# Kernel optimization log

Measured on AMD Instinct MI355X. Metric: run time of the kernel, lower is better.

The kernel has to match this reference:

```python
import jax, jax.numpy as jnp
import numpy as np

DIM = 768
B, N = 16, 1024
EPS_LN = 1e-5

def _layernorm(x, gamma, beta):
    mu = jnp.mean(x, axis=-1, keepdims=True)
    var = jnp.mean((x - mu) ** 2, axis=-1, keepdims=True)
    return (x - mu) * jax.lax.rsqrt(var + EPS_LN) * gamma + beta

def _gelu(x):
    return jax.nn.gelu(x, approximate=False)

def setup_inputs() -> dict:
    key = jax.random.key(0)
    ks = jax.random.split(key, 10)
    d = DIM
    s1 = 1.0 / np.sqrt(2 * d)
    s = 1.0 / np.sqrt(d)
    return {
        "x": jax.random.normal(ks[0], (B, N, d), dtype=jnp.float32),
        "gamma": jnp.ones((d,), jnp.float32),
        "beta": jnp.zeros((d,), jnp.float32),
        "w1": jax.random.normal(ks[1], (2 * d, d), jnp.float32) * s1,
        "b1": jnp.zeros((d,), jnp.float32),
        "w2": jax.random.normal(ks[2], (d, d), jnp.float32) * s,
        "b2": jnp.zeros((d,), jnp.float32),
        "w3": jax.random.normal(ks[3], (d, d), jnp.float32) * s,
        "b3": jnp.zeros((d,), jnp.float32),
        "w4": jax.random.normal(ks[4], (d, d), jnp.float32) * s,
        "b4": jnp.zeros((d,), jnp.float32),
    }

def reference(x, gamma, beta, w1, b1, w2, b2, w3, b3, w4, b4):
    # x: [B, N, D]
    avg_x = jnp.mean(x, axis=1)                      # [B, D]
    A = avg_x[:, None, :] * jax.nn.sigmoid(_layernorm(x, gamma, beta))  # [B, N, D]
    # batched pairwise Euclidean distance among tokens (replaces python loop)
    sq = jnp.sum(A * A, axis=-1)                     # [B, N]
    d2 = sq[:, :, None] + sq[:, None, :] - 2.0 * jnp.einsum('bnd,bmd->bnm', A, A)
    dist = jnp.sqrt(jnp.clip(d2, 1e-12))             # [B, N, N]
    m = jnp.max(dist, axis=-1)                       # [B, N]
    m_x = x + m[..., None]                           # [B, N, D]
    cat = jnp.concatenate([A, m_x], axis=-1)         # [B, N, 2D]
    m1 = _gelu(cat @ w1 + b1)                        # layer1
    W = _gelu(m1 @ w2 + b2)                          # layer2
    Wdyn = x * W
    l3 = _gelu((m1 * Wdyn) @ w3 + b3)                # layer3
    out = _gelu((x * l3) @ w4 + b4)                  # layer4
    return out.astype(jnp.float32)
```

## Files before the change

kernel.cpp:

```cpp
#include <hip/hip_runtime.h>
#include <hip/hip_fp16.h>
#include <math.h>

#define DIM 768
#define NTOK 1024
#define NBATCH 16
#define BNR (NBATCH * NTOK)

typedef _Float16 f16x8 __attribute__((ext_vector_type(8)));
typedef float f32x4 __attribute__((ext_vector_type(4)));

__device__ __forceinline__ void gl2lds16(const void* g, void* l) {
    __builtin_amdgcn_global_load_lds(
        (const __attribute__((address_space(1))) void*)g,
        (__attribute__((address_space(3))) void*)l, 16, 0, 0);
}

__device__ __forceinline__ float gelu_fast(float z) {
    const float s = z * 0.70710678118654752f;
    const float ax = fabsf(s);
    const float t = __builtin_amdgcn_rcpf(1.0f + 0.3275911f * ax);
    const float poly = t * (0.254829592f + t * (-0.284496736f +
                       t * (1.421413741f + t * (-1.453152027f + t * 1.061405429f))));
    const float e = __expf(-ax * ax);
    float erfv = 1.0f - poly * e;
    erfv = copysignf(erfv, s);
    return 0.5f * z * (1.0f + erfv);
}

__device__ __forceinline__ float block_sum(float v, float* sbuf) {
    #pragma unroll
    for (int o = 32; o > 0; o >>= 1) v += __shfl_down(v, o, 64);
    const int lane = threadIdx.x & 63, w = threadIdx.x >> 6;
    if (lane == 0) sbuf[w] = v;
    __syncthreads();
    const float r = sbuf[0] + sbuf[1] + sbuf[2] + sbuf[3];
    __syncthreads();
    return r;
}

__global__ __launch_bounds__(256) void avg_kernel(const float* __restrict__ x,
                                                  float* __restrict__ avgx) {
    const int d = blockIdx.x * 256 + threadIdx.x;
    const int b = blockIdx.y;
    const int n0 = blockIdx.z * 128;
    const float* xp = x + (size_t)b * NTOK * DIM + (size_t)n0 * DIM + d;
    float s = 0.0f;
    for (int n = 0; n < 128; ++n) s += xp[(size_t)n * DIM];
    atomicAdd(&avgx[b * DIM + d], s * (1.0f / NTOK));
}

__global__ __launch_bounds__(256) void ln_sig_kernel(
    const float* __restrict__ x, const float* __restrict__ gamma,
    const float* __restrict__ beta, const float* __restrict__ avgx,
    __half* __restrict__ Ah, float* __restrict__ sq)
{
    __shared__ float sbuf[4];
    const int row = blockIdx.x;
    const int b = row >> 10;
    const int tid = threadIdx.x;
    const float* xr = x + (size_t)row * DIM;
    float v[3];
    #pragma unroll
    for (int i = 0; i < 3; ++i) v[i] = xr[tid + 256 * i];
    const float mu = block_sum(v[0] + v[1] + v[2], sbuf) * (1.0f / DIM);
    float ss = 0.0f;
    #pragma unroll
    for (int i = 0; i < 3; ++i) { const float d = v[i] - mu; ss += d * d; }
    const float var = block_sum(ss, sbuf) * (1.0f / DIM);
    const float rstd = rsqrtf(var + 1e-5f);
    const float* ag = avgx + b * DIM;
    float qs = 0.0f;
    #pragma unroll
    for (int i = 0; i < 3; ++i) {
        const int d = tid + 256 * i;
        const float ln = (v[i] - mu) * rstd * gamma[d] + beta[d];
        const float sg = 1.0f / (1.0f + expf(-ln));
        const float a = ag[d] * sg;
        const __half h = __float2half(a);
        const float ar = __half2float(h);
        Ah[(size_t)row * DIM + d] = h;
        qs += ar * ar;
    }
    const float tot = block_sum(qs, sbuf);
    if (tid == 0) sq[row] = tot;
}

__global__ __launch_bounds__(256) void wconv(const float* __restrict__ w,
                                             __half* __restrict__ wT, int K, int N)
{
    __shared__ float t[64][65];
    const int k0 = blockIdx.y * 64, n0 = blockIdx.x * 64;
    const int tid = threadIdx.x;
    const int r = tid >> 4, c4 = (tid & 15) * 4;
    #pragma unroll
    for (int p = 0; p < 4; ++p) {
        const int rr = p * 16 + r;
        const float4 v = *(const float4*)&w[(size_t)(k0 + rr) * N + n0 + c4];
        t[rr][c4] = v.x; t[rr][c4 + 1] = v.y; t[rr][c4 + 2] = v.z; t[rr][c4 + 3] = v.w;
    }
    __syncthreads();
    #pragma unroll
    for (int p = 0; p < 4; ++p) {
        const int nn = p * 16 + r;
        ushort4 pk;
        pk.x = __half_as_ushort(__float2half(t[c4 + 0][nn]));
        pk.y = __half_as_ushort(__float2half(t[c4 + 1][nn]));
        pk.z = __half_as_ushort(__float2half(t[c4 + 2][nn]));
        pk.w = __half_as_ushort(__float2half(t[c4 + 3][nn]));
        *(ushort4*)&wT[(size_t)(n0 + nn) * K + k0 + c4] = pk;
    }
}

__global__ __launch_bounds__(256) void xm_kernel(const float* __restrict__ x,
                                                 const float* __restrict__ m,
                                                 __half* __restrict__ xmH) {
    const int row = blockIdx.x;
    const float mv = m[row];
    #pragma unroll
    for (int i = 0; i < 3; ++i) {
        const int d = threadIdx.x + i * 256;
        xmH[(size_t)row * DIM + d] = __float2half(x[(size_t)row * DIM + d] + mv);
    }
}

template<int K, bool CAT, int EPI>
__global__ __launch_bounds__(256, 4) void gemm16(
    const __half* __restrict__ A0, const __half* __restrict__ A1,
    const __half* __restrict__ BT, const float* __restrict__ bias,
    const float* __restrict__ xin, const __half* __restrict__ m1h,
    __half* __restrict__ outH, float* __restrict__ outF)
{
    __shared__ _Float16 As0[128 * 32];
    __shared__ _Float16 Bs0[128 * 32];
    __shared__ _Float16 As1[128 * 32];
    __shared__ _Float16 Bs1[128 * 32];
    const int tid = threadIdx.x;
    const int w = tid >> 6, lane = tid & 63;
    const int wu = __builtin_amdgcn_readfirstlane(w);
    const int wr = w >> 1, wc = w & 1;
    const int R0 = blockIdx.x * 128, J0 = blockIdx.y * 128;
    constexpr int rs = CAT ? DIM : K;
    const int srow = lane >> 2;
    const int sk8 = (((lane & 3) ^ ((lane >> 2) & 3))) * 8;
    const int fx = ((lane >> 4) ^ (lane & 3)) * 8;
    constexpr int NT = K / 32;
    static_assert(NT % 2 == 0, "two-phase loop needs even NT");

    f32x4 acc[4][4];
    #pragma unroll
    for (int mt = 0; mt < 4; ++mt)
        #pragma unroll
        for (int nt = 0; nt < 4; ++nt) {
            f32x4 z = {0.0f, 0.0f, 0.0f, 0.0f};
            acc[mt][nt] = z;
        }

    auto stage = [&](_Float16 (&Asb)[128 * 32], _Float16 (&Bsb)[128 * 32], int k0) {
        const __half* Ab = (CAT && k0 >= DIM) ? (A1 + (k0 - DIM)) : (A0 + k0);
        #pragma unroll
        for (int i = 0; i < 2; ++i) {
            const int rbase = i * 64 + w * 16;
            const int rbu = i * 64 + wu * 16;
            gl2lds16(Ab + (size_t)(R0 + rbase + srow) * rs + sk8, &Asb[rbu * 32]);
            gl2lds16(BT + (size_t)(J0 + rbase + srow) * K + k0 + sk8, &Bsb[rbu * 32]);
        }
    };
    auto rdfrags = [&](const _Float16 (&Asb)[128 * 32], const _Float16 (&Bsb)[128 * 32],
                       f16x8* af, f16x8* bf) {
        #pragma unroll
        for (int mt = 0; mt < 4; ++mt)
            af[mt] = *(const f16x8*)&Asb[(wr * 64 + mt * 16 + (lane & 15)) * 32 + fx];
        #pragma unroll
        for (int nt = 0; nt < 4; ++nt)
            bf[nt] = *(const f16x8*)&Bsb[(wc * 64 + nt * 16 + (lane & 15)) * 32 + fx];
    };
    auto domfma = [&](const f16x8* af, const f16x8* bf) {
        #pragma unroll
        for (int mt = 0; mt < 4; ++mt)
            #pragma unroll
            for (int nt = 0; nt < 4; ++nt)
                acc[mt][nt] = __builtin_amdgcn_mfma_f32_16x16x32_f16(af[mt], bf[nt], acc[mt][nt], 0, 0, 0);
    };

    stage(As0, Bs0, 0);
    __syncthreads();
    for (int kt = 0; kt < NT; kt += 2) {
        f16x8 af[4], bf[4];
        rdfrags(As0, Bs0, af, bf);
        stage(As1, Bs1, (kt + 1) * 32);
        domfma(af, bf);
        __syncthreads();
        rdfrags(As1, Bs1, af, bf);
        if (kt + 2 < NT) stage(As0, Bs0, (kt + 2) * 32);
        domfma(af, bf);
        __syncthreads();
    }

    #pragma unroll
    for (int mt = 0; mt < 4; ++mt) {
        #pragma unroll
        for (int nt = 0; nt < 4; ++nt) {
            const int col = J0 + wc * 64 + nt * 16 + (lane & 15);
            const float bv = bias[col];
            #pragma unroll
            for (int r = 0; r < 4; ++r) {
                const int row = R0 + wr * 64 + mt * 16 + (lane >> 4) * 4 + r;
                const size_t off = (size_t)row * DIM + col;
                const float g = gelu_fast(acc[mt][nt][r] + bv);
                if (EPI == 0) {
                    outH[off] = __float2half(g);
                } else if (EPI == 1) {
                    outH[off] = __float2half(__half2float(m1h[off]) * xin[off] * g);
                } else if (EPI == 2) {
                    outH[off] = __float2half(xin[off] * g);
                } else {
                    outF[off] = g;
                }
            }
        }
    }
}

__global__ __launch_bounds__(256, 4) void dist16(const __half* __restrict__ Ah,
                                                 const float* __restrict__ sq,
                                                 float* __restrict__ m)
{
    __shared__ _Float16 As0[128 * 32];
    __shared__ _Float16 Bs0[128 * 32];
    __shared__ _Float16 As1[128 * 32];
    __shared__ _Float16 Bs1[128 * 32];
    const int tid = threadIdx.x;
    const int w = tid >> 6, lane = tid & 63;
    const int wu = __builtin_amdgcn_readfirstlane(w);
    const int wr = w >> 1, wc = w & 1;
    const int base = blockIdx.x * NTOK;
    const int I0 = blockIdx.y * 128, J0 = blockIdx.z * 128;
    const int srow = lane >> 2;
    const int sk8 = (((lane & 3) ^ ((lane >> 2) & 3))) * 8;
    const int fx = ((lane >> 4) ^ (lane & 3)) * 8;
    constexpr int NT = DIM / 32;

    f32x4 acc[4][4];
    #pragma unroll
    for (int mt = 0; mt < 4; ++mt)
        #pragma unroll
        for (int nt = 0; nt < 4; ++nt) {
            f32x4 z = {0.0f, 0.0f, 0.0f, 0.0f};
            acc[mt][nt] = z;
        }

    auto stage = [&](_Float16 (&Asb)[128 * 32], _Float16 (&Bsb)[128 * 32], int k0) {
        #pragma unroll
        for (int i = 0; i < 2; ++i) {
            const int rbase = i * 64 + w * 16;
            const int rbu = i * 64 + wu * 16;
            gl2lds16(Ah + (size_t)(base + I0 + rbase + srow) * DIM + k0 + sk8, &Asb[rbu * 32]);
            gl2lds16(Ah + (size_t)(base + J0 + rbase + srow) * DIM + k0 + sk8, &Bsb[rbu * 32]);
        }
    };
    auto rdfrags = [&](const _Float16 (&Asb)[128 * 32], const _Float16 (&Bsb)[128 * 32],
                       f16x8* af, f16x8* bf) {
        #pragma unroll
        for (int mt = 0; mt < 4; ++mt)
            af[mt] = *(const f16x8*)&Asb[(wr * 64 + mt * 16 + (lane & 15)) * 32 + fx];
        #pragma unroll
        for (int nt = 0; nt < 4; ++nt)
            bf[nt] = *(const f16x8*)&Bsb[(wc * 64 + nt * 16 + (lane & 15)) * 32 + fx];
    };
    auto domfma = [&](const f16x8* af, const f16x8* bf) {
        #pragma unroll
        for (int mt = 0; mt < 4; ++mt)
            #pragma unroll
            for (int nt = 0; nt < 4; ++nt)
                acc[mt][nt] = __builtin_amdgcn_mfma_f32_16x16x32_f16(af[mt], bf[nt], acc[mt][nt], 0, 0, 0);
    };

    stage(As0, Bs0, 0);
    __syncthreads();
    for (int kt = 0; kt < NT; kt += 2) {
        f16x8 af[4], bf[4];
        rdfrags(As0, Bs0, af, bf);
        stage(As1, Bs1, (kt + 1) * 32);
        domfma(af, bf);
        __syncthreads();
        rdfrags(As1, Bs1, af, bf);
        if (kt + 2 < NT) stage(As0, Bs0, (kt + 2) * 32);
        domfma(af, bf);
        __syncthreads();
    }

    #pragma unroll
    for (int mt = 0; mt < 4; ++mt) {
        float sqi[4];
        #pragma unroll
        for (int r = 0; r < 4; ++r)
            sqi[r] = sq[base + I0 + wr * 64 + mt * 16 + (lane >> 4) * 4 + r];
        float vmax[4] = {-1e30f, -1e30f, -1e30f, -1e30f};
        #pragma unroll
        for (int nt = 0; nt < 4; ++nt) {
            const float sqj = sq[base + J0 + wc * 64 + nt * 16 + (lane & 15)];
            #pragma unroll
            for (int r = 0; r < 4; ++r)
                vmax[r] = fmaxf(vmax[r], sqi[r] + sqj - 2.0f * acc[mt][nt][r]);
        }
        #pragma unroll
        for (int r = 0; r < 4; ++r) {
            float v = vmax[r];
            v = fmaxf(v, __shfl_xor(v, 1, 64));
            v = fmaxf(v, __shfl_xor(v, 2, 64));
            v = fmaxf(v, __shfl_xor(v, 4, 64));
            v = fmaxf(v, __shfl_xor(v, 8, 64));
            if ((lane & 15) == 0) {
                const float d = sqrtf(fmaxf(v, 1e-12f));
                atomicMax((unsigned int*)&m[base + I0 + wr * 64 + mt * 16 + (lane >> 4) * 4 + r],
                          __float_as_uint(d));
            }
        }
    }
}

extern "C" void kernel_launch(void* const* d_in, const int* in_sizes, int n_in,
                              void* d_out, int out_size, void* d_ws, size_t ws_size,
                              hipStream_t stream)
{
    const float* x     = (const float*)d_in[0];
    const float* gamma = (const float*)d_in[1];
    const float* beta  = (const float*)d_in[2];
    const float* w1    = (const float*)d_in[3];
    const float* b1    = (const float*)d_in[4];
    const float* w2    = (const float*)d_in[5];
    const float* b2    = (const float*)d_in[6];
    const float* w3    = (const float*)d_in[7];
    const float* b3    = (const float*)d_in[8];
    const float* w4    = (const float*)d_in[9];
    const float* b4    = (const float*)d_in[10];
    float* out = (float*)d_out;
    float* ws  = (float*)d_ws;

    float* avgx = ws;
    float* sq   = ws + 12288;
    float* mbuf = sq + 16384;
    __half* w1T = (__half*)(mbuf + 16384);
    __half* w2T = w1T + (size_t)1536 * 768;
    __half* w3T = w2T + (size_t)768 * 768;
    __half* w4T = w3T + (size_t)768 * 768;
    __half* P0  = w4T + (size_t)768 * 768;
    __half* P1  = P0 + (size_t)BNR * DIM;
    __half* Ah  = (__half*)d_out;
    __half* xmH = Ah + (size_t)BNR * DIM;

    hipMemsetAsync(avgx, 0, 12288 * sizeof(float), stream);
    hipMemsetAsync(mbuf, 0, BNR * sizeof(float), stream);
    wconv<<<dim3(12, 24), 256, 0, stream>>>(w1, w1T, 1536, 768);
    wconv<<<dim3(12, 12), 256, 0, stream>>>(w2, w2T, 768, 768);
    wconv<<<dim3(12, 12), 256, 0, stream>>>(w3, w3T, 768, 768);
    wconv<<<dim3(12, 12), 256, 0, stream>>>(w4, w4T, 768, 768);
    avg_kernel<<<dim3(3, NBATCH, 8), 256, 0, stream>>>(x, avgx);
    ln_sig_kernel<<<BNR, 256, 0, stream>>>(x, gamma, beta, avgx, Ah, sq);
    dist16<<<dim3(NBATCH, 8, 8), 256, 0, stream>>>(Ah, sq, mbuf);
    xm_kernel<<<BNR, 256, 0, stream>>>(x, mbuf, xmH);
    gemm16<1536, true, 0><<<dim3(128, 6), 256, 0, stream>>>(
        Ah, xmH, w1T, b1, nullptr, nullptr, P0, nullptr);
    gemm16<768, false, 1><<<dim3(128, 6), 256, 0, stream>>>(
        P0, nullptr, w2T, b2, x, P0, P1, nullptr);
    gemm16<768, false, 2><<<dim3(128, 6), 256, 0, stream>>>(
        P1, nullptr, w3T, b3, x, nullptr, P0, nullptr);
    gemm16<768, false, 3><<<dim3(128, 6), 256, 0, stream>>>(
        P0, nullptr, w4T, b4, x, nullptr, nullptr, out);
}
```

Before: 359.8 us.

## Retile MLP GEMMs to 64x128 tiles with BK=64 single-buffered LDS

Changes the four MLP GEMM kernels from 128x128 tiles with BK=32 double-buffered LDS to 64x128 tiles with BK=64 and a single LDS buffer. It uses a new XOR swizzle on 8-element octets and doubles the grid along rows. Occupancy hint rises to 6 blocks per CU. The aim is more blocks for better CU fill and fewer barriers per K step. In exchange it loses the prefetch overlap of global loads with MFMA and reuses each B tile over fewer A rows.

```diff
diff --git a/kernel.cpp b/kernel.cpp
--- a/kernel.cpp
+++ b/kernel.cpp
@@ -125,87 +125,83 @@
 }
 
 template<int K, bool CAT, int EPI>
-__global__ __launch_bounds__(256, 4) void gemm16(
+__global__ __launch_bounds__(256, 6) void gemm16(
     const __half* __restrict__ A0, const __half* __restrict__ A1,
     const __half* __restrict__ BT, const float* __restrict__ bias,
     const float* __restrict__ xin, const __half* __restrict__ m1h,
     __half* __restrict__ outH, float* __restrict__ outF)
 {
-    __shared__ _Float16 As0[128 * 32];
-    __shared__ _Float16 Bs0[128 * 32];
-    __shared__ _Float16 As1[128 * 32];
-    __shared__ _Float16 Bs1[128 * 32];
+    __shared__ _Float16 As[64 * 64];
+    __shared__ _Float16 Bs[128 * 64];
     const int tid = threadIdx.x;
     const int w = tid >> 6, lane = tid & 63;
     const int wu = __builtin_amdgcn_readfirstlane(w);
     const int wr = w >> 1, wc = w & 1;
-    const int R0 = blockIdx.x * 128, J0 = blockIdx.y * 128;
+    const int R0 = blockIdx.x * 64, J0 = blockIdx.y * 128;
     constexpr int rs = CAT ? DIM : K;
-    const int srow = lane >> 2;
-    const int sk8 = (((lane & 3) ^ ((lane >> 2) & 3))) * 8;
-    const int fx = ((lane >> 4) ^ (lane & 3)) * 8;
-    constexpr int NT = K / 32;
-    static_assert(NT % 2 == 0, "two-phase loop needs even NT");
-
-    f32x4 acc[4][4];
-    #pragma unroll
-    for (int mt = 0; mt < 4; ++mt)
+    const int srow = lane >> 3;
+    const int soct = (lane & 7) ^ ((lane >> 3) & 7);
+    constexpr int NT = K / 64;
+    static_assert(K % 64 == 0, "BK=64 requires K % 64 == 0");
+
+    f32x4 acc[2][4];
+    #pragma unroll
+    for (int mt = 0; mt < 2; ++mt)
         #pragma unroll
         for (int nt = 0; nt < 4; ++nt) {
             f32x4 z = {0.0f, 0.0f, 0.0f, 0.0f};
             acc[mt][nt] = z;
         }
 
-    auto stage = [&](_Float16 (&Asb)[128 * 32], _Float16 (&Bsb)[128 * 32], int k0) {
+    for (int kt = 0; kt < NT; ++kt) {
+        const int k0 = kt * 64;
         const __half* Ab = (CAT && k0 >= DIM) ? (A1 + (k0 - DIM)) : (A0 + k0);
         #pragma unroll
         for (int i = 0; i < 2; ++i) {
-            const int rbase = i * 64 + w * 16;
-            const int rbu = i * 64 + wu * 16;
-            gl2lds16(Ab + (size_t)(R0 + rbase + srow) * rs + sk8, &Asb[rbu * 32]);
-            gl2lds16(BT + (size_t)(J0 + rbase + srow) * K + k0 + sk8, &Bsb[rbu * 32]);
-        }
-    };
-    auto rdfrags = [&](const _Float16 (&Asb)[128 * 32], const _Float16 (&Bsb)[128 * 32],
-                       f16x8* af, f16x8* bf) {
-        #pragma unroll
-        for (int mt = 0; mt < 4; ++mt)
-            af[mt] = *(const f16x8*)&Asb[(wr * 64 + mt * 16 + (lane & 15)) * 32 + fx];
-        #pragma unroll
-        for (int nt = 0; nt < 4; ++nt)
-            bf[nt] = *(const f16x8*)&Bsb[(wc * 64 + nt * 16 + (lane & 15)) * 32 + fx];
-    };
-    auto domfma = [&](const f16x8* af, const f16x8* bf) {
-        #pragma unroll
-        for (int mt = 0; mt < 4; ++mt)
-            #pragma unroll
-            for (int nt = 0; nt < 4; ++nt)
-                acc[mt][nt] = __builtin_amdgcn_mfma_f32_16x16x32_f16(af[mt], bf[nt], acc[mt][nt], 0, 0, 0);
-    };
-
-    stage(As0, Bs0, 0);
-    __syncthreads();
-    for (int kt = 0; kt < NT; kt += 2) {
-        f16x8 af[4], bf[4];
-        rdfrags(As0, Bs0, af, bf);
-        stage(As1, Bs1, (kt + 1) * 32);
-        domfma(af, bf);
+            const int row = (2 * w + i) * 8 + srow;
+            gl2lds16(Ab + (size_t)(R0 + row) * rs + soct * 8, &As[(2 * wu + i) * 512]);
+        }
+        #pragma unroll
+        for (int i = 0; i < 4; ++i) {
+            const int row = (4 * w + i) * 8 + srow;
+            gl2lds16(BT + (size_t)(J0 + row) * K + k0 + soct * 8, &Bs[(4 * wu + i) * 512]);
+        }
         __syncthreads();
-        rdfrags(As1, Bs1, af, bf);
-        if (kt + 2 < NT) stage(As0, Bs0, (kt + 2) * 32);
-        domfma(af, bf);
+        f16x8 af[2][2], bf[2][4];
+        #pragma unroll
+        for (int h = 0; h < 2; ++h) {
+            #pragma unroll
+            for (int mt = 0; mt < 2; ++mt) {
+                const int arow = wr * 32 + mt * 16 + (lane & 15);
+                const int o = h * 4 + (lane >> 4);
+                af[h][mt] = *(const f16x8*)&As[arow * 64 + ((o ^ (arow & 7)) * 8)];
+            }
+            #pragma unroll
+            for (int nt = 0; nt < 4; ++nt) {
+                const int brow = wc * 64 + nt * 16 + (lane & 15);
+                const int o = h * 4 + (lane >> 4);
+                bf[h][nt] = *(const f16x8*)&Bs[brow * 64 + ((o ^ (brow & 7)) * 8)];
+            }
+        }
+        #pragma unroll
+        for (int h = 0; h < 2; ++h)
+            #pragma unroll
+            for (int mt = 0; mt < 2; ++mt)
+                #pragma unroll
+                for (int nt = 0; nt < 4; ++nt)
+                    acc[mt][nt] = __builtin_amdgcn_mfma_f32_16x16x32_f16(af[h][mt], bf[h][nt], acc[mt][nt], 0, 0, 0);
         __syncthreads();
     }
 
     #pragma unroll
-    for (int mt = 0; mt < 4; ++mt) {
+    for (int mt = 0; mt < 2; ++mt) {
         #pragma unroll
         for (int nt = 0; nt < 4; ++nt) {
             const int col = J0 + wc * 64 + nt * 16 + (lane & 15);
             const float bv = bias[col];
             #pragma unroll
             for (int r = 0; r < 4; ++r) {
-                const int row = R0 + wr * 64 + mt * 16 + (lane >> 4) * 4 + r;
+                const int row = R0 + wr * 32 + mt * 16 + (lane >> 4) * 4 + r;
                 const size_t off = (size_t)row * DIM + col;
                 const float g = gelu_fast(acc[mt][nt][r] + bv);
                 if (EPI == 0) {
@@ -360,12 +356,12 @@
     ln_sig_kernel<<<BNR, 256, 0, stream>>>(x, gamma, beta, avgx, Ah, sq);
     dist16<<<dim3(NBATCH, 8, 8), 256, 0, stream>>>(Ah, sq, mbuf);
     xm_kernel<<<BNR, 256, 0, stream>>>(x, mbuf, xmH);
-    gemm16<1536, true, 0><<<dim3(128, 6), 256, 0, stream>>>(
+    gemm16<1536, true, 0><<<dim3(256, 6), 256, 0, stream>>>(
         Ah, xmH, w1T, b1, nullptr, nullptr, P0, nullptr);
-    gemm16<768, false, 1><<<dim3(128, 6), 256, 0, stream>>>(
+    gemm16<768, false, 1><<<dim3(256, 6), 256, 0, stream>>>(
         P0, nullptr, w2T, b2, x, P0, P1, nullptr);
-    gemm16<768, false, 2><<<dim3(128, 6), 256, 0, stream>>>(
+    gemm16<768, false, 2><<<dim3(256, 6), 256, 0, stream>>>(
         P1, nullptr, w3T, b3, x, nullptr, P0, nullptr);
-    gemm16<768, false, 3><<<dim3(128, 6), 256, 0, stream>>>(
+    gemm16<768, false, 3><<<dim3(256, 6), 256, 0, stream>>>(
         P0, nullptr, w4T, b4, x, nullptr, nullptr, out);
 }
```

New measurement: 422.5 us. 1.17x slower.
